# Performance work log

Measured on AMD Instinct MI355X. Metric: run time of the kernel, lower is better.

Reference implementation:

```python
import jax, jax.numpy as jnp
import numpy as np

B, V, N, C = 32, 5, 196, 768
H = 768          # hidden_dim of score MLP
NUM_ITERS = 3


def setup_inputs() -> dict:
    key = jax.random.key(0)
    ks = jax.random.split(key, 6)
    scale = 1.0 / np.sqrt(C)
    x = jax.random.normal(ks[0], (B, V, N, C), dtype=jnp.float32)
    # per-view projection weights, stacked: [V, C, C] (no bias)
    w_views = jax.random.uniform(ks[1], (V, C, C), dtype=jnp.float32, minval=-scale, maxval=scale)
    # score MLP: Linear(2C -> H), Tanh, Linear(H -> 1)
    s1 = 1.0 / np.sqrt(2 * C)
    w1 = jax.random.uniform(ks[2], (2 * C, H), dtype=jnp.float32, minval=-s1, maxval=s1)
    b1 = jax.random.uniform(ks[3], (H,), dtype=jnp.float32, minval=-s1, maxval=s1)
    s2 = 1.0 / np.sqrt(H)
    w2 = jax.random.uniform(ks[4], (H, 1), dtype=jnp.float32, minval=-s2, maxval=s2)
    b2 = jax.random.uniform(ks[5], (1,), dtype=jnp.float32, minval=-s2, maxval=s2)
    return {"x": x, "w_views": w_views, "w1": w1, "b1": b1, "w2": w2, "b2": b2}


def reference(x, w_views, w1, b1, w2, b2):
    # x: [B, V, N, C]
    c = x.mean(axis=1)                                   # [B, N, C]
    # per-view projections are independent of c: compute once (same math)
    proj_x = jnp.einsum('bvnc,vcd->bvnd', x, w_views)    # [B, V, N, C]
    a = None
    for _ in range(NUM_ITERS):
        c_exp = jnp.broadcast_to(c[:, None], x.shape)    # [B, V, N, C]
        si = jnp.concatenate([x, c_exp], axis=-1)        # [B, V, N, 2C]
        h = jnp.tanh(jnp.einsum('bvnk,kh->bvnh', si, w1) + b1)
        s = (jnp.einsum('bvnh,ho->bvno', h, w2) + b2)[..., 0]  # [B, V, N]
        a = jax.nn.softmax(s, axis=1)                    # softmax over views
        c = jnp.einsum('bvn,bvnc->bnc', a, proj_x)       # weighted sum over V
    eps = 1e-8
    entropy = -(a * jnp.log(a + eps)).sum(axis=1)        # [B, N]
    r = 1.0 - entropy / np.log(V)
    return c, r
```

## Files before the change

### kernel.cpp

```cpp
#include <hip/hip_runtime.h>

#define CDIM   768
#define NSEQ   196
#define NVIEW  5
#define BN_TOT 6272
#define SLAB   4816896
#define WSLAB  589824

typedef __attribute__((ext_vector_type(8))) short short8;
typedef __attribute__((ext_vector_type(4))) float f32x4;

__device__ __forceinline__ float bf_lo(unsigned u) { return __uint_as_float(u << 16); }
__device__ __forceinline__ float bf_hi(unsigned u) { return __uint_as_float(u & 0xffff0000u); }
__device__ __forceinline__ unsigned short f2bf(float f) {
  unsigned u = __float_as_uint(f);
  return (unsigned short)((u + 0x7fffu + ((u >> 16) & 1u)) >> 16);
}
__device__ __forceinline__ unsigned pack2(float f0, float f1) {
  return (unsigned)f2bf(f0) | ((unsigned)f2bf(f1) << 16);
}
__device__ __forceinline__ float ftanh(float x) {
  x = fminf(fmaxf(x, -10.f), 10.f);
  float e = __expf(2.f * x);
  return (e - 1.f) / (e + 1.f);
}
__device__ __forceinline__ void async_cp16(const void* g, void* l) {
  __builtin_amdgcn_global_load_lds((const __attribute__((address_space(1))) unsigned*)g,
                                   (__attribute__((address_space(3))) unsigned*)l, 16, 0, 0);
}

__global__ __launch_bounds__(256) void k_tr(const float* __restrict__ wv,
                                            const float* __restrict__ w1,
                                            unsigned short* __restrict__ wvT,
                                            unsigned short* __restrict__ w1aT,
                                            unsigned short* __restrict__ w1bT) {
  __shared__ float tile[32][33];
  const int m = blockIdx.z;
  const float* src;
  unsigned short* dst;
  if (m < NVIEW)      { src = wv + (size_t)m * WSLAB; dst = wvT + (size_t)m * WSLAB; }
  else if (m == NVIEW){ src = w1;                     dst = w1aT; }
  else                { src = w1 + WSLAB;             dst = w1bT; }
  const int tx = threadIdx.x, ty = threadIdx.y;
  const int x0 = blockIdx.x * 32, y0 = blockIdx.y * 32;
#pragma unroll
  for (int i = 0; i < 4; ++i)
    tile[ty + i * 8][tx] = src[(size_t)(y0 + ty + i * 8) * CDIM + x0 + tx];
  __syncthreads();
#pragma unroll
  for (int i = 0; i < 4; ++i)
    dst[(size_t)(x0 + ty + i * 8) * CDIM + y0 + tx] = f2bf(tile[tx][ty + i * 8]);
}

__global__ __launch_bounds__(192) void k_cvt_mean(const float* __restrict__ x,
                                                  unsigned short* __restrict__ xb,
                                                  unsigned short* __restrict__ cb) {
  const int bn = blockIdx.x;
  const int b = bn / NSEQ, n = bn % NSEQ;
  const int h = threadIdx.x * 4;
  const float* xp = x + ((size_t)(b * NVIEW) * NSEQ + n) * CDIM + h;
  float s0 = 0, s1 = 0, s2 = 0, s3 = 0;
#pragma unroll
  for (int v = 0; v < NVIEW; ++v) {
    float4 p = *(const float4*)(xp + (size_t)v * (NSEQ * CDIM));
    s0 += p.x; s1 += p.y; s2 += p.z; s3 += p.w;
    uint2 q; q.x = pack2(p.x, p.y); q.y = pack2(p.z, p.w);
    *(uint2*)(xb + ((size_t)v * BN_TOT + bn) * CDIM + h) = q;
  }
  uint2 o;
  o.x = pack2(s0 * 0.2f, s1 * 0.2f);
  o.y = pack2(s2 * 0.2f, s3 * 0.2f);
  *(uint2*)(cb + (size_t)bn * CDIM + h) = o;
}

template <int MODE>
__global__ __launch_bounds__(256) void gemm_bt(const unsigned short* __restrict__ P0,
                                               const unsigned short* __restrict__ P1,
                                               const unsigned short* __restrict__ P2,
                                               unsigned short* __restrict__ Q0,
                                               unsigned short* __restrict__ Q1) {
  __shared__ __align__(16) unsigned short ldsA[128 * 32];
  __shared__ __align__(16) unsigned short ldsB[128 * 32];
  const int t = threadIdx.x;
  const int w = t >> 6, lane = t & 63;
  const int lr = lane & 15, lq = lane >> 4;
  const int wm = (w >> 1) * 64, wn = (w & 1) * 64;
  const int mt = blockIdx.y, z = blockIdx.z;
  int nt = blockIdx.x;
  const unsigned short *A, *Bt;
  unsigned short* C;
  if (MODE == 0) {
    A = P0 + (size_t)z * SLAB;
    if (nt < 6) { Bt = P1 + (size_t)z * WSLAB; C = Q0 + (size_t)z * SLAB; }
    else        { Bt = P2;                     C = Q1 + (size_t)z * SLAB; nt -= 6; }
  } else {
    Bt = P2;
    if (z < NVIEW) { A = P0 + (size_t)z * SLAB; C = Q0 + (size_t)z * SLAB; }
    else           { A = P1;                    C = Q1; }
  }

  const unsigned short* ga0 = A + ((size_t)mt * 128 + (t >> 2)) * CDIM + (t & 3) * 8;
  const unsigned short* ga1 = ga0 + (size_t)64 * CDIM;
  const unsigned short* gb0 = Bt + ((size_t)nt * 128 + (t >> 2)) * CDIM + (t & 3) * 8;
  const unsigned short* gb1 = gb0 + (size_t)64 * CDIM;

  f32x4 acc[4][4] = {};
  for (int k0 = 0; k0 < CDIM; k0 += 32) {
    __syncthreads();
    async_cp16(ga0 + k0, &ldsA[w * 512]);
    async_cp16(ga1 + k0, &ldsA[2048 + w * 512]);
    async_cp16(gb0 + k0, &ldsB[w * 512]);
    async_cp16(gb1 + k0, &ldsB[2048 + w * 512]);
    __syncthreads();
    short8 af[4], bv[4];
#pragma unroll
    for (int i = 0; i < 4; ++i) af[i] = *(const short8*)&ldsA[(wm + i * 16 + lr) * 32 + lq * 8];
#pragma unroll
    for (int j = 0; j < 4; ++j) bv[j] = *(const short8*)&ldsB[(wn + j * 16 + lr) * 32 + lq * 8];
#pragma unroll
    for (int i = 0; i < 4; ++i)
#pragma unroll
      for (int j = 0; j < 4; ++j)
        acc[i][j] = __builtin_amdgcn_mfma_f32_16x16x32_bf16(af[i], bv[j], acc[i][j], 0, 0, 0);
  }
#pragma unroll
  for (int i = 0; i < 4; ++i)
#pragma unroll
    for (int j = 0; j < 4; ++j) {
      const int gc = nt * 128 + wn + j * 16 + lr;
      const int gr = mt * 128 + wm + i * 16 + lq * 4;
#pragma unroll
      for (int r = 0; r < 4; ++r)
        C[(size_t)(gr + r) * CDIM + gc] = f2bf(acc[i][j][r]);
    }
}

__global__ __launch_bounds__(192) void k_iter(const unsigned short* __restrict__ xw1b,
                                              unsigned short* __restrict__ cw1,
                                              const unsigned short* __restrict__ pw,
                                              const float* __restrict__ b1,
                                              const float* __restrict__ w2,
                                              float* __restrict__ outc,
                                              float* __restrict__ outr, int last) {
  __shared__ float red[3][NVIEW];
  __shared__ float aa[NVIEW];
  const int bn = blockIdx.x;
  const int t = threadIdx.x, wv_ = t >> 6, lane = t & 63;
  const int h = t * 4;

  uint2 cv = *(const uint2*)(cw1 + (size_t)bn * CDIM + h);
  float4 bv = *(const float4*)(b1 + h);
  float4 w2v = *(const float4*)(w2 + h);
  const float c0 = bf_lo(cv.x) + bv.x, c1 = bf_hi(cv.x) + bv.y;
  const float c2 = bf_lo(cv.y) + bv.z, c3 = bf_hi(cv.y) + bv.w;

  float part[NVIEW];
#pragma unroll
  for (int v = 0; v < NVIEW; ++v) {
    uint2 xv = *(const uint2*)(xw1b + ((size_t)v * BN_TOT + bn) * CDIM + h);
    float p;
    p  = w2v.x * ftanh(bf_lo(xv.x) + c0);
    p  = fmaf(w2v.y, ftanh(bf_hi(xv.x) + c1), p);
    p  = fmaf(w2v.z, ftanh(bf_lo(xv.y) + c2), p);
    p  = fmaf(w2v.w, ftanh(bf_hi(xv.y) + c3), p);
    part[v] = p;
  }
#pragma unroll
  for (int off = 32; off > 0; off >>= 1)
#pragma unroll
    for (int v = 0; v < NVIEW; ++v) part[v] += __shfl_down(part[v], off);
  if (lane == 0)
#pragma unroll
    for (int v = 0; v < NVIEW; ++v) red[wv_][v] = part[v];
  __syncthreads();
  if (t == 0) {
    float s[NVIEW];
#pragma unroll
    for (int v = 0; v < NVIEW; ++v) s[v] = red[0][v] + red[1][v] + red[2][v];
    float m = s[0];
#pragma unroll
    for (int v = 1; v < NVIEW; ++v) m = fmaxf(m, s[v]);
    float a[NVIEW], sum = 0.f;
#pragma unroll
    for (int v = 0; v < NVIEW; ++v) { a[v] = __expf(s[v] - m); sum += a[v]; }
    const float inv = 1.f / sum;
#pragma unroll
    for (int v = 0; v < NVIEW; ++v) { a[v] *= inv; aa[v] = a[v]; }
    if (last) {
      float ent = 0.f;
#pragma unroll
      for (int v = 0; v < NVIEW; ++v) ent -= a[v] * logf(a[v] + 1e-8f);
      outr[bn] = 1.f - ent * 0.6213349345596119f;
    }
  }
  __syncthreads();

  float a0 = aa[0], a1 = aa[1], a2 = aa[2], a3 = aa[3], a4 = aa[4];
  float r0 = 0, r1 = 0, r2 = 0, r3 = 0;
#pragma unroll
  for (int v = 0; v < NVIEW; ++v) {
    const float av = (v == 0) ? a0 : (v == 1) ? a1 : (v == 2) ? a2 : (v == 3) ? a3 : a4;
    uint2 p = *(const uint2*)(pw + ((size_t)v * BN_TOT + bn) * CDIM + h);
    r0 = fmaf(av, bf_lo(p.x), r0); r1 = fmaf(av, bf_hi(p.x), r1);
    r2 = fmaf(av, bf_lo(p.y), r2); r3 = fmaf(av, bf_hi(p.y), r3);
  }
  if (!last) {
    uint2 o; o.x = pack2(r0, r1); o.y = pack2(r2, r3);
    *(uint2*)(cw1 + (size_t)bn * CDIM + h) = o;
  } else {
    float4 of; of.x = r0; of.y = r1; of.z = r2; of.w = r3;
    *(float4*)(outc + (size_t)bn * CDIM + h) = of;
  }
}

extern "C" void kernel_launch(void* const* d_in, const int* in_sizes, int n_in,
                              void* d_out, int out_size, void* d_ws, size_t ws_size,
                              hipStream_t stream) {
  (void)in_sizes; (void)n_in; (void)out_size; (void)ws_size;
  const float* x  = (const float*)d_in[0];
  const float* wv = (const float*)d_in[1];
  const float* w1 = (const float*)d_in[2];
  const float* b1 = (const float*)d_in[3];
  const float* w2 = (const float*)d_in[4];

  unsigned short* ws   = (unsigned short*)d_ws;
  unsigned short* wvT  = ws;
  unsigned short* w1aT = ws + 2949120;
  unsigned short* w1bT = ws + 3538944;
  unsigned short* xb   = ws + 4128768;
  unsigned short* projb= ws + 28213248;
  unsigned short* xw1b = ws + 52297728;
  unsigned short* pw1b = ws + 76382208;
  unsigned short* cb   = ws + 100466688;
  unsigned short* cw1  = ws + 105283584;

  float* outc = (float*)d_out;
  float* outr = outc + SLAB;

  k_tr<<<dim3(24, 24, 7), dim3(32, 8), 0, stream>>>(wv, w1, wvT, w1aT, w1bT);
  k_cvt_mean<<<BN_TOT, 192, 0, stream>>>(x, xb, cb);
  gemm_bt<0><<<dim3(12, 49, NVIEW), 256, 0, stream>>>(xb, wvT, w1aT, projb, xw1b);
  gemm_bt<1><<<dim3(6, 49, NVIEW + 1), 256, 0, stream>>>(projb, cb, w1bT, pw1b, cw1);
  k_iter<<<BN_TOT, 192, 0, stream>>>(xw1b, cw1, pw1b, b1, w2, outc, outr, 0);
  k_iter<<<BN_TOT, 192, 0, stream>>>(xw1b, cw1, pw1b, b1, w2, outc, outr, 0);
  k_iter<<<BN_TOT, 192, 0, stream>>>(xw1b, cw1, projb, b1, w2, outc, outr, 1);
}
```

Baseline: 405.1 us.

## Fuse paired GEMMs sharing an operand and merge three iteration kernels into one

```diff
diff --git a/kernel.cpp b/kernel.cpp
--- a/kernel.cpp
+++ b/kernel.cpp
@@ -74,54 +74,66 @@
 }
 
 template <int MODE>
-__global__ __launch_bounds__(256) void gemm_bt(const unsigned short* __restrict__ P0,
-                                               const unsigned short* __restrict__ P1,
-                                               const unsigned short* __restrict__ P2,
-                                               unsigned short* __restrict__ Q0,
-                                               unsigned short* __restrict__ Q1) {
-  __shared__ __align__(16) unsigned short ldsA[128 * 32];
-  __shared__ __align__(16) unsigned short ldsB[128 * 32];
-  const int t = threadIdx.x;
-  const int w = t >> 6, lane = t & 63;
+__global__ __launch_bounds__(256) void gemm_dual(const unsigned short* __restrict__ P0,
+                                                 const unsigned short* __restrict__ P1,
+                                                 const unsigned short* __restrict__ P2,
+                                                 unsigned short* __restrict__ Q0,
+                                                 unsigned short* __restrict__ Q1) {
+  __shared__ __align__(16) unsigned short ldsX[128 * 32];
+  __shared__ __align__(16) unsigned short ldsY[128 * 32];
+  __shared__ __align__(16) unsigned short ldsZ[128 * 32];
+  const int t = threadIdx.x, w = t >> 6, lane = t & 63;
   const int lr = lane & 15, lq = lane >> 4;
   const int wm = (w >> 1) * 64, wn = (w & 1) * 64;
-  const int mt = blockIdx.y, z = blockIdx.z;
-  int nt = blockIdx.x;
-  const unsigned short *A, *Bt;
-  unsigned short* C;
+  const int nt = blockIdx.x, mt = blockIdx.y, z = blockIdx.z;
+  const unsigned short *g0, *g1, *g2;
+  unsigned short *C0, *C1;
   if (MODE == 0) {
-    A = P0 + (size_t)z * SLAB;
-    if (nt < 6) { Bt = P1 + (size_t)z * WSLAB; C = Q0 + (size_t)z * SLAB; }
-    else        { Bt = P2;                     C = Q1 + (size_t)z * SLAB; nt -= 6; }
+    g0 = P0 + (size_t)z * SLAB;
+    g1 = P1 + (size_t)z * WSLAB;
+    g2 = P2;
+    C0 = Q0 + (size_t)z * SLAB;
+    C1 = Q1 + (size_t)z * SLAB;
   } else {
-    Bt = P2;
-    if (z < NVIEW) { A = P0 + (size_t)z * SLAB; C = Q0 + (size_t)z * SLAB; }
-    else           { A = P1;                    C = Q1; }
-  }
-
-  const unsigned short* ga0 = A + ((size_t)mt * 128 + (t >> 2)) * CDIM + (t & 3) * 8;
-  const unsigned short* ga1 = ga0 + (size_t)64 * CDIM;
-  const unsigned short* gb0 = Bt + ((size_t)nt * 128 + (t >> 2)) * CDIM + (t & 3) * 8;
-  const unsigned short* gb1 = gb0 + (size_t)64 * CDIM;
-
-  f32x4 acc[4][4] = {};
+    g0 = P0 + (size_t)(2 * z) * SLAB;
+    g1 = P2;
+    g2 = (z < 2) ? P0 + (size_t)(2 * z + 1) * SLAB : P1;
+    C0 = Q0 + (size_t)(2 * z) * SLAB;
+    C1 = (z < 2) ? Q0 + (size_t)(2 * z + 1) * SLAB : Q1;
+  }
+  const int r2 = (MODE == 0) ? nt : mt;
+  const unsigned short* p0 = g0 + ((size_t)mt * 128 + (t >> 2)) * CDIM + (t & 3) * 8;
+  const unsigned short* p1 = g1 + ((size_t)nt * 128 + (t >> 2)) * CDIM + (t & 3) * 8;
+  const unsigned short* p2 = g2 + ((size_t)r2 * 128 + (t >> 2)) * CDIM + (t & 3) * 8;
+
+  f32x4 acc0[4][4] = {}, acc1[4][4] = {};
   for (int k0 = 0; k0 < CDIM; k0 += 32) {
     __syncthreads();
-    async_cp16(ga0 + k0, &ldsA[w * 512]);
-    async_cp16(ga1 + k0, &ldsA[2048 + w * 512]);
-    async_cp16(gb0 + k0, &ldsB[w * 512]);
-    async_cp16(gb1 + k0, &ldsB[2048 + w * 512]);
-    __syncthreads();
-    short8 af[4], bv[4];
-#pragma unroll
-    for (int i = 0; i < 4; ++i) af[i] = *(const short8*)&ldsA[(wm + i * 16 + lr) * 32 + lq * 8];
-#pragma unroll
-    for (int j = 0; j < 4; ++j) bv[j] = *(const short8*)&ldsB[(wn + j * 16 + lr) * 32 + lq * 8];
+    async_cp16(p0 + k0, &ldsX[w * 512]);
+    async_cp16(p0 + (size_t)64 * CDIM + k0, &ldsX[2048 + w * 512]);
+    async_cp16(p1 + k0, &ldsY[w * 512]);
+    async_cp16(p1 + (size_t)64 * CDIM + k0, &ldsY[2048 + w * 512]);
+    async_cp16(p2 + k0, &ldsZ[w * 512]);
+    async_cp16(p2 + (size_t)64 * CDIM + k0, &ldsZ[2048 + w * 512]);
+    __syncthreads();
+    short8 fx[4], fy[4], fz[4];
+#pragma unroll
+    for (int i = 0; i < 4; ++i) fx[i] = *(const short8*)&ldsX[(wm + i * 16 + lr) * 32 + lq * 8];
+#pragma unroll
+    for (int j = 0; j < 4; ++j) fy[j] = *(const short8*)&ldsY[(wn + j * 16 + lr) * 32 + lq * 8];
+#pragma unroll
+    for (int j = 0; j < 4; ++j)
+      fz[j] = *(const short8*)&ldsZ[(((MODE == 0 ? wn : wm) + j * 16 + lr)) * 32 + lq * 8];
 #pragma unroll
     for (int i = 0; i < 4; ++i)
 #pragma unroll
-      for (int j = 0; j < 4; ++j)
-        acc[i][j] = __builtin_amdgcn_mfma_f32_16x16x32_bf16(af[i], bv[j], acc[i][j], 0, 0, 0);
+      for (int j = 0; j < 4; ++j) {
+        acc0[i][j] = __builtin_amdgcn_mfma_f32_16x16x32_bf16(fx[i], fy[j], acc0[i][j], 0, 0, 0);
+        if (MODE == 0)
+          acc1[i][j] = __builtin_amdgcn_mfma_f32_16x16x32_bf16(fx[i], fz[j], acc1[i][j], 0, 0, 0);
+        else
+          acc1[i][j] = __builtin_amdgcn_mfma_f32_16x16x32_bf16(fz[i], fy[j], acc1[i][j], 0, 0, 0);
+      }
   }
 #pragma unroll
   for (int i = 0; i < 4; ++i)
@@ -130,86 +142,101 @@
       const int gc = nt * 128 + wn + j * 16 + lr;
       const int gr = mt * 128 + wm + i * 16 + lq * 4;
 #pragma unroll
-      for (int r = 0; r < 4; ++r)
-        C[(size_t)(gr + r) * CDIM + gc] = f2bf(acc[i][j][r]);
-    }
-}
-
-__global__ __launch_bounds__(192) void k_iter(const unsigned short* __restrict__ xw1b,
-                                              unsigned short* __restrict__ cw1,
-                                              const unsigned short* __restrict__ pw,
-                                              const float* __restrict__ b1,
-                                              const float* __restrict__ w2,
-                                              float* __restrict__ outc,
-                                              float* __restrict__ outr, int last) {
+      for (int r = 0; r < 4; ++r) {
+        C0[(size_t)(gr + r) * CDIM + gc] = f2bf(acc0[i][j][r]);
+        C1[(size_t)(gr + r) * CDIM + gc] = f2bf(acc1[i][j][r]);
+      }
+    }
+}
+
+__global__ __launch_bounds__(192) void k_iter3(const unsigned short* __restrict__ xw1b,
+                                               const unsigned short* __restrict__ cw1,
+                                               const unsigned short* __restrict__ pw1b,
+                                               const unsigned short* __restrict__ projb,
+                                               const float* __restrict__ b1,
+                                               const float* __restrict__ w2,
+                                               float* __restrict__ outc,
+                                               float* __restrict__ outr) {
   __shared__ float red[3][NVIEW];
   __shared__ float aa[NVIEW];
-  const int bn = blockIdx.x;
-  const int t = threadIdx.x, wv_ = t >> 6, lane = t & 63;
+  const int bn = blockIdx.x, t = threadIdx.x, wid = t >> 6, lane = t & 63;
   const int h = t * 4;
-
-  uint2 cv = *(const uint2*)(cw1 + (size_t)bn * CDIM + h);
-  float4 bv = *(const float4*)(b1 + h);
-  float4 w2v = *(const float4*)(w2 + h);
-  const float c0 = bf_lo(cv.x) + bv.x, c1 = bf_hi(cv.x) + bv.y;
-  const float c2 = bf_lo(cv.y) + bv.z, c3 = bf_hi(cv.y) + bv.w;
-
-  float part[NVIEW];
+  const float4 bv = *(const float4*)(b1 + h);
+  const float4 wv = *(const float4*)(w2 + h);
+  float cw[4];
+  { uint2 c = *(const uint2*)(cw1 + (size_t)bn * CDIM + h);
+    cw[0] = bf_lo(c.x); cw[1] = bf_hi(c.x); cw[2] = bf_lo(c.y); cw[3] = bf_hi(c.y); }
+  float xw[NVIEW][4], pf[NVIEW][4];
 #pragma unroll
   for (int v = 0; v < NVIEW; ++v) {
-    uint2 xv = *(const uint2*)(xw1b + ((size_t)v * BN_TOT + bn) * CDIM + h);
-    float p;
-    p  = w2v.x * ftanh(bf_lo(xv.x) + c0);
-    p  = fmaf(w2v.y, ftanh(bf_hi(xv.x) + c1), p);
-    p  = fmaf(w2v.z, ftanh(bf_lo(xv.y) + c2), p);
-    p  = fmaf(w2v.w, ftanh(bf_hi(xv.y) + c3), p);
-    part[v] = p;
-  }
-#pragma unroll
-  for (int off = 32; off > 0; off >>= 1)
-#pragma unroll
-    for (int v = 0; v < NVIEW; ++v) part[v] += __shfl_down(part[v], off);
-  if (lane == 0)
-#pragma unroll
-    for (int v = 0; v < NVIEW; ++v) red[wv_][v] = part[v];
-  __syncthreads();
-  if (t == 0) {
-    float s[NVIEW];
-#pragma unroll
-    for (int v = 0; v < NVIEW; ++v) s[v] = red[0][v] + red[1][v] + red[2][v];
-    float m = s[0];
-#pragma unroll
-    for (int v = 1; v < NVIEW; ++v) m = fmaxf(m, s[v]);
-    float a[NVIEW], sum = 0.f;
-#pragma unroll
-    for (int v = 0; v < NVIEW; ++v) { a[v] = __expf(s[v] - m); sum += a[v]; }
-    const float inv = 1.f / sum;
-#pragma unroll
-    for (int v = 0; v < NVIEW; ++v) { a[v] *= inv; aa[v] = a[v]; }
-    if (last) {
-      float ent = 0.f;
-#pragma unroll
-      for (int v = 0; v < NVIEW; ++v) ent -= a[v] * logf(a[v] + 1e-8f);
-      outr[bn] = 1.f - ent * 0.6213349345596119f;
-    }
-  }
-  __syncthreads();
-
-  float a0 = aa[0], a1 = aa[1], a2 = aa[2], a3 = aa[3], a4 = aa[4];
-  float r0 = 0, r1 = 0, r2 = 0, r3 = 0;
-#pragma unroll
-  for (int v = 0; v < NVIEW; ++v) {
-    const float av = (v == 0) ? a0 : (v == 1) ? a1 : (v == 2) ? a2 : (v == 3) ? a3 : a4;
-    uint2 p = *(const uint2*)(pw + ((size_t)v * BN_TOT + bn) * CDIM + h);
-    r0 = fmaf(av, bf_lo(p.x), r0); r1 = fmaf(av, bf_hi(p.x), r1);
-    r2 = fmaf(av, bf_lo(p.y), r2); r3 = fmaf(av, bf_hi(p.y), r3);
-  }
-  if (!last) {
-    uint2 o; o.x = pack2(r0, r1); o.y = pack2(r2, r3);
-    *(uint2*)(cw1 + (size_t)bn * CDIM + h) = o;
-  } else {
-    float4 of; of.x = r0; of.y = r1; of.z = r2; of.w = r3;
-    *(float4*)(outc + (size_t)bn * CDIM + h) = of;
+    uint2 q = *(const uint2*)(xw1b + ((size_t)v * BN_TOT + bn) * CDIM + h);
+    xw[v][0] = bf_lo(q.x) + bv.x; xw[v][1] = bf_hi(q.x) + bv.y;
+    xw[v][2] = bf_lo(q.y) + bv.z; xw[v][3] = bf_hi(q.y) + bv.w;
+    uint2 p = *(const uint2*)(pw1b + ((size_t)v * BN_TOT + bn) * CDIM + h);
+    pf[v][0] = bf_lo(p.x); pf[v][1] = bf_hi(p.x);
+    pf[v][2] = bf_lo(p.y); pf[v][3] = bf_hi(p.y);
+  }
+  for (int it = 0; it < 3; ++it) {
+    float part[NVIEW];
+#pragma unroll
+    for (int v = 0; v < NVIEW; ++v) {
+      float p;
+      p = wv.x * ftanh(xw[v][0] + cw[0]);
+      p = fmaf(wv.y, ftanh(xw[v][1] + cw[1]), p);
+      p = fmaf(wv.z, ftanh(xw[v][2] + cw[2]), p);
+      p = fmaf(wv.w, ftanh(xw[v][3] + cw[3]), p);
+      part[v] = p;
+    }
+#pragma unroll
+    for (int off = 32; off > 0; off >>= 1)
+#pragma unroll
+      for (int v = 0; v < NVIEW; ++v) part[v] += __shfl_down(part[v], off);
+    if (lane == 0)
+#pragma unroll
+      for (int v = 0; v < NVIEW; ++v) red[wid][v] = part[v];
+    __syncthreads();
+    if (t == 0) {
+      float s[NVIEW];
+#pragma unroll
+      for (int v = 0; v < NVIEW; ++v) s[v] = red[0][v] + red[1][v] + red[2][v];
+      float m = s[0];
+#pragma unroll
+      for (int v = 1; v < NVIEW; ++v) m = fmaxf(m, s[v]);
+      float a[NVIEW], sum = 0.f;
+#pragma unroll
+      for (int v = 0; v < NVIEW; ++v) { a[v] = __expf(s[v] - m); sum += a[v]; }
+      const float inv = 1.f / sum;
+#pragma unroll
+      for (int v = 0; v < NVIEW; ++v) { a[v] *= inv; aa[v] = a[v]; }
+      if (it == 2) {
+        float ent = 0.f;
+#pragma unroll
+        for (int v = 0; v < NVIEW; ++v) ent -= a[v] * logf(a[v] + 1e-8f);
+        outr[bn] = 1.f - ent * 0.6213349345596119f;
+      }
+    }
+    __syncthreads();
+    if (it < 2) {
+      float n0 = 0, n1 = 0, n2 = 0, n3 = 0;
+#pragma unroll
+      for (int v = 0; v < NVIEW; ++v) {
+        const float av = aa[v];
+        n0 = fmaf(av, pf[v][0], n0); n1 = fmaf(av, pf[v][1], n1);
+        n2 = fmaf(av, pf[v][2], n2); n3 = fmaf(av, pf[v][3], n3);
+      }
+      cw[0] = n0; cw[1] = n1; cw[2] = n2; cw[3] = n3;
+    } else {
+      float r0 = 0, r1 = 0, r2 = 0, r3 = 0;
+#pragma unroll
+      for (int v = 0; v < NVIEW; ++v) {
+        const float av = aa[v];
+        uint2 p = *(const uint2*)(projb + ((size_t)v * BN_TOT + bn) * CDIM + h);
+        r0 = fmaf(av, bf_lo(p.x), r0); r1 = fmaf(av, bf_hi(p.x), r1);
+        r2 = fmaf(av, bf_lo(p.y), r2); r3 = fmaf(av, bf_hi(p.y), r3);
+      }
+      float4 of; of.x = r0; of.y = r1; of.z = r2; of.w = r3;
+      *(float4*)(outc + (size_t)bn * CDIM + h) = of;
+    }
   }
 }
 
@@ -239,9 +266,7 @@
 
   k_tr<<<dim3(24, 24, 7), dim3(32, 8), 0, stream>>>(wv, w1, wvT, w1aT, w1bT);
   k_cvt_mean<<<BN_TOT, 192, 0, stream>>>(x, xb, cb);
-  gemm_bt<0><<<dim3(12, 49, NVIEW), 256, 0, stream>>>(xb, wvT, w1aT, projb, xw1b);
-  gemm_bt<1><<<dim3(6, 49, NVIEW + 1), 256, 0, stream>>>(projb, cb, w1bT, pw1b, cw1);
-  k_iter<<<BN_TOT, 192, 0, stream>>>(xw1b, cw1, pw1b, b1, w2, outc, outr, 0);
-  k_iter<<<BN_TOT, 192, 0, stream>>>(xw1b, cw1, pw1b, b1, w2, outc, outr, 0);
-  k_iter<<<BN_TOT, 192, 0, stream>>>(xw1b, cw1, projb, b1, w2, outc, outr, 1);
-}
+  gemm_dual<0><<<dim3(6, 49, NVIEW), 256, 0, stream>>>(xb, wvT, w1aT, projb, xw1b);
+  gemm_dual<1><<<dim3(6, 49, 3), 256, 0, stream>>>(projb, cb, w1bT, pw1b, cw1);
+  k_iter3<<<BN_TOT, 192, 0, stream>>>(xw1b, cw1, pw1b, projb, b1, w2, outc, outr);
+}
```

Result: slower. 496.0 us (+22.5%).
